# Performance work log

Hardware: AMD Instinct MI355X
Metric: run time of the kernel (lower is better)

The kernel has to match this reference:

```python
import jax, jax.numpy as jnp
import numpy as np

EPS = 1e-5  # torch LayerNorm default

def _std(x):
    # standardize over the last 3 (tensor-feature) modes, biased variance like torch LayerNorm
    mu = jnp.mean(x, axis=(-3, -2, -1), keepdims=True)
    var = jnp.mean(jnp.square(x - mu), axis=(-3, -2, -1), keepdims=True)
    return (x - mu) * jax.lax.rsqrt(var + EPS)

def setup_inputs() -> dict:
    key = jax.random.key(0)
    ks = jax.random.split(key, 12)
    T, B = 512, 16
    a = b = c = 16          # input tensor modes (4096 features)
    ha = hb = hc = 8        # hidden tensor modes (512 features)
    G = 3                   # gates: r, z, n
    f32 = jnp.float32
    return {
        "x": jax.random.normal(ks[0], (T, B, a, b, c), f32),
        "h0": jnp.zeros((B, ha, hb, hc), f32),
        # input-to-hidden TCL3D factors + rank-1 bias + LN affines (stacked over 3 gates)
        "W_fa": jax.random.normal(ks[1], (G, a, ha), f32),
        "W_fb": jax.random.normal(ks[2], (G, b, hb), f32),
        "W_fc": jax.random.normal(ks[3], (G, c, hc), f32),
        "W_ba": jax.random.normal(ks[4], (G, ha), f32),
        "W_bb": jax.random.normal(ks[5], (G, hb), f32),
        "W_bc": jax.random.normal(ks[6], (G, hc), f32),
        "W_lnin_w": jnp.ones((G, a, b, c), f32),
        "W_lnin_b": jnp.zeros((G, a, b, c), f32),
        "W_lnout_w": jnp.ones((G, ha, hb, hc), f32),
        "W_lnout_b": jnp.zeros((G, ha, hb, hc), f32),
        # hidden-to-hidden TCL3D factors + rank-1 bias + LN affines
        "U_fa": jax.random.normal(ks[7], (G, ha, ha), f32),
        "U_fb": jax.random.normal(ks[8], (G, hb, hb), f32),
        "U_fc": jax.random.normal(ks[9], (G, hc, hc), f32),
        "U_ba": jax.random.normal(ks[10], (G, ha), f32),
        "U_bb": jax.random.normal(ks[11], (G, hb), f32),
        "U_bc": jax.random.normal(jax.random.fold_in(key, 99), (G, hc), f32),
        "U_lnin_w": jnp.ones((G, ha, hb, hc), f32),
        "U_lnin_b": jnp.zeros((G, ha, hb, hc), f32),
        "U_lnout_w": jnp.ones((G, ha, hb, hc), f32),
        "U_lnout_b": jnp.zeros((G, ha, hb, hc), f32),
    }

def reference(x, h0, W_fa, W_fb, W_fc, W_ba, W_bb, W_bc,
              W_lnin_w, W_lnin_b, W_lnout_w, W_lnout_b,
              U_fa, U_fb, U_fc, U_ba, U_bb, U_bc,
              U_lnin_w, U_lnin_b, U_lnout_w, U_lnout_b):
    # --- input-to-hidden TCL3D for all 3 gates, batched over time (no h dependence) ---
    xh = _std(x)                                                  # [T,B,a,b,c]
    xg = xh[None] * W_lnin_w[:, None, None] + W_lnin_b[:, None, None]  # [3,T,B,a,b,c]
    Wx = jnp.einsum('gtnabc,gad,gbe,gcf->gtndef', xg, W_fa, W_fb, W_fc)
    Wx = Wx + (W_ba[:, None, None, :, None, None]
               * W_bb[:, None, None, None, :, None]
               * W_bc[:, None, None, None, None, :])              # rank-1 bias
    Wx = _std(Wx) * W_lnout_w[:, None, None] + W_lnout_b[:, None, None]
    Wx = jnp.swapaxes(Wx, 0, 1)                                   # [T,3,B,ha,hb,hc]

    Ub = (U_ba[:, None, :, None, None]
          * U_bb[:, None, None, :, None]
          * U_bc[:, None, None, None, :])                         # [3,1,ha,hb,hc]

    def step(h, wx):
        # hidden-to-hidden TCL3D for all 3 gates
        hh = _std(h)                                              # [B,ha,hb,hc]
        hg = hh[None] * U_lnin_w[:, None] + U_lnin_b[:, None]     # [3,B,ha,hb,hc]
        Uh = jnp.einsum('gndef,gdp,geq,gfr->gnpqr', hg, U_fa, U_fb, U_fc) + Ub
        Uh = _std(Uh) * U_lnout_w[:, None] + U_lnout_b[:, None]
        r = jax.nn.sigmoid(wx[0] + Uh[0])
        z = jax.nn.sigmoid(wx[1] + Uh[1])
        n = jnp.tanh(wx[2] + r * Uh[2])
        h_new = (1.0 - z) * n + z * h
        return h_new, h_new

    _, outs = jax.lax.scan(step, h0, Wx)                          # [T,B,ha,hb,hc]
    return outs
```

## Files before the change

### kernel.cpp

```cpp
#include <hip/hip_runtime.h>

#define EPSV 1e-5f

#define DPP_XADD(v, ctrl)                                                  \
    v += __int_as_float(__builtin_amdgcn_update_dpp(                       \
        0, __float_as_int(v), ctrl, 0xF, 0xF, false))

__device__ __forceinline__ float wave_allsum(float v) {
    DPP_XADD(v, 0x128);
    DPP_XADD(v, 0x124);
    DPP_XADD(v, 0x122);
    DPP_XADD(v, 0x121);
    DPP_XADD(v, 0x142);
    DPP_XADD(v, 0x143);
    return __int_as_float(__builtin_amdgcn_readlane(__float_as_int(v), 63));
}

__global__ __launch_bounds__(256) void wx_kernel(
    const float* __restrict__ x,
    const float* __restrict__ Wfa, const float* __restrict__ Wfb,
    const float* __restrict__ Wfc,
    const float* __restrict__ Wba, const float* __restrict__ Wbb,
    const float* __restrict__ Wbc,
    const float* __restrict__ lniw, const float* __restrict__ lnib,
    const float* __restrict__ lnow, const float* __restrict__ lnob,
    float* __restrict__ wxo)
{
    __shared__ float Xs[4096];
    __shared__ float S1[2048];
    __shared__ float S2[1024];
    __shared__ float baS[24], bbS[24], bcS[24];
    __shared__ float red[16];

    const int tid  = threadIdx.x;
    const int wid  = tid >> 6, lane = tid & 63;
    const size_t tb = blockIdx.x;
    const float* xp = x + tb * 4096;

    float s = 0.f, s2 = 0.f;
    for (int i = tid; i < 4096; i += 256) {
        float v = xp[i];
        Xs[i] = v;
        s += v; s2 += v * v;
    }
    if (tid < 24) { baS[tid] = Wba[tid]; bbS[tid] = Wbb[tid]; bcS[tid] = Wbc[tid]; }

    __syncthreads();
    #pragma unroll
    for (int off = 32; off > 0; off >>= 1) {
        s  += __shfl_down(s,  off);
        s2 += __shfl_down(s2, off);
    }
    if (lane == 0) { red[wid] = s; red[8 + wid] = s2; }
    __syncthreads();
    s  = red[0] + red[1] + red[2] + red[3];
    s2 = red[8] + red[9] + red[10] + red[11];
    const float muX = s * (1.f / 4096.f);
    const float rsX = rsqrtf(fmaxf(s2 * (1.f / 4096.f) - muX * muX, 0.f) + EPSV);

    const int qh = __builtin_amdgcn_readfirstlane(tid >> 7);
    const int rh = __builtin_amdgcn_readfirstlane(tid >> 6);

    for (int g = 0; g < 3; ++g) {
        {
            float acc[8] = {0,0,0,0,0,0,0,0};
            const int rest = tid;
            const float* lw = lniw + g * 4096;
            const float* lb = lnib + g * 4096;
            #pragma unroll
            for (int m = 0; m < 16; ++m) {
                const float xn = (Xs[m*256 + rest] - muX) * rsX;
                const float xv = fmaf(xn, lw[m*256 + rest], lb[m*256 + rest]);
                #pragma unroll
                for (int p = 0; p < 8; ++p)
                    acc[p] = fmaf(xv, Wfa[(g*16 + m)*8 + p], acc[p]);
            }
            #pragma unroll
            for (int p = 0; p < 8; ++p)
                S1[p*256 + (rest ^ (p << 3))] = acc[p];
        }
        __syncthreads();
        {
            float acc[4] = {0,0,0,0};
            const int rest2 = tid & 127;
            const int c2 = rest2 >> 3, p2 = rest2 & 7;
            #pragma unroll
            for (int m = 0; m < 16; ++m) {
                const float xv = S1[p2*256 + (((m << 4) | c2) ^ (p2 << 3))];
                #pragma unroll
                for (int j = 0; j < 4; ++j)
                    acc[j] = fmaf(xv, Wfb[(g*16 + m)*8 + qh*4 + j], acc[j]);
            }
            #pragma unroll
            for (int j = 0; j < 4; ++j) {
                const int q = qh*4 + j;
                S2[q*128 + (rest2 ^ (q << 3))] = acc[j];
            }
        }
        __syncthreads();
        float v0, v1; int idx0;
        {
            float acc[2] = {0, 0};
            const int rest3 = tid & 63;
            const int q3 = rest3 & 7, pp = rest3 >> 3;
            #pragma unroll
            for (int m = 0; m < 16; ++m) {
                const float xv = S2[q3*128 + (((m << 3) | pp) ^ (q3 << 3))];
                #pragma unroll
                for (int j = 0; j < 2; ++j)
                    acc[j] = fmaf(xv, Wfc[(g*16 + m)*8 + rh*2 + j], acc[j]);
            }
            const float bpq = baS[g*8 + pp] * bbS[g*8 + q3];
            v0 = acc[0] + bpq * bcS[g*8 + rh*2 + 0];
            v1 = acc[1] + bpq * bcS[g*8 + rh*2 + 1];
            idx0 = rest3 * 8 + rh * 2;
        }
        float t = v0 + v1, t2 = v0*v0 + v1*v1;
        __syncthreads();
        #pragma unroll
        for (int off = 32; off > 0; off >>= 1) {
            t  += __shfl_down(t,  off);
            t2 += __shfl_down(t2, off);
        }
        if (lane == 0) { red[wid] = t; red[8 + wid] = t2; }
        __syncthreads();
        t  = red[0] + red[1] + red[2] + red[3];
        t2 = red[8] + red[9] + red[10] + red[11];
        const float mu  = t * (1.f / 512.f);
        const float var = fmaxf(t2 * (1.f / 512.f) - mu * mu, 0.f);
        const float rs  = rsqrtf(var + EPSV);
        float* wp = wxo + (tb * 3 + g) * 512;
        const float2 lw2 = *(const float2*)(lnow + g*512 + idx0);
        const float2 lb2 = *(const float2*)(lnob + g*512 + idx0);
        float2 o2;
        o2.x = fmaf((v0 - mu) * rs, lw2.x, lb2.x);
        o2.y = fmaf((v1 - mu) * rs, lw2.y, lb2.y);
        *(float2*)(wp + idx0) = o2;
    }
}

__global__ __launch_bounds__(192, 1) void scan_kernel(
    const float* __restrict__ wx,
    const float* __restrict__ h0,
    const float* __restrict__ Ufa, const float* __restrict__ Ufb,
    const float* __restrict__ Ufc,
    const float* __restrict__ Uba, const float* __restrict__ Ubb,
    const float* __restrict__ Ubc,
    const float* __restrict__ lniw, const float* __restrict__ lnib,
    const float* __restrict__ lnow, const float* __restrict__ lnob,
    float* __restrict__ out,
    int T, int B)
{
    const int n    = blockIdx.x;
    const int tid  = threadIdx.x;
    const int lane = tid & 63;
    const int gu   = __builtin_amdgcn_readfirstlane(tid >> 6);

    __shared__ float hgS[3][512];
    __shared__ float T1S[3][512];
    __shared__ float T2S[3][512];
    __shared__ float UhS[2][3][512];

    const float* __restrict__ WA = Ufa + gu * 64;
    const float* __restrict__ WB = Ufb + gu * 64;
    const float* __restrict__ WC = Ufc + gu * 64;

    float lnw[8], lnb[8], low8[8], lob8[8], ub[8];
    {
        const int p_ = lane >> 3, q_ = lane & 7;
        const float bpq = Uba[gu*8 + p_] * Ubb[gu*8 + q_];
        #pragma unroll
        for (int k = 0; k < 8; ++k) {
            lnw[k]  = lniw[gu*512 + lane*8 + k];
            lnb[k]  = lnib[gu*512 + lane*8 + k];
            low8[k] = lnow[gu*512 + lane*8 + k];
            lob8[k] = lnob[gu*512 + lane*8 + k];
            ub[k]   = bpq * Ubc[gu*8 + k];
        }
    }

    int wb[8], rb2[8];
    #pragma unroll
    for (int j = 0; j < 8; ++j) wb[j] = j*64 + (lane ^ (j << 2));
    {
        const int c = lane & 7, r = lane >> 3;
        #pragma unroll
        for (int m = 0; m < 8; ++m)
            rb2[m] = c*64 + (((m << 3) | r) ^ (c << 2));
    }

    float hv[8];
    {
        const float4 a = *(const float4*)(h0 + n*512 + lane*8);
        const float4 b = *(const float4*)(h0 + n*512 + lane*8 + 4);
        hv[0]=a.x; hv[1]=a.y; hv[2]=a.z; hv[3]=a.w;
        hv[4]=b.x; hv[5]=b.y; hv[6]=b.z; hv[7]=b.w;
    }

    float pf[3][8];
#define LOADWX(TT)                                                         \
    {                                                                      \
        const float* base_ = wx + (((size_t)(TT) * B + n) * 3) * 512       \
                             + lane * 8;                                   \
        _Pragma("unroll")                                                  \
        for (int gg = 0; gg < 3; ++gg) {                                   \
            const float4 A_ = *(const float4*)(base_ + gg*512);            \
            const float4 B_ = *(const float4*)(base_ + gg*512 + 4);       \
            pf[gg][0]=A_.x; pf[gg][1]=A_.y; pf[gg][2]=A_.z; pf[gg][3]=A_.w;\
            pf[gg][4]=B_.x; pf[gg][5]=B_.y; pf[gg][6]=B_.z; pf[gg][7]=B_.w;\
        }                                                                  \
    }

#define STAGE(INBUF, WPTR, AOUT)                                           \
    _Pragma("unroll")                                                      \
    for (int m = 0; m < 8; ++m) {                                          \
        const float xv = INBUF[gu][rb2[m]];                                \
        _Pragma("unroll")                                                  \
        for (int q = 0; q < 8; ++q)                                        \
            AOUT[q] = fmaf(xv, WPTR[m*8 + q], AOUT[q]);                    \
    }

#define PIPELINE(PAR)                                                      \
    {                                                                      \
        float sA = 0.f, sB = 0.f;                                          \
        _Pragma("unroll")                                                  \
        for (int k = 0; k < 8; ++k) { sA += hv[k]; sB += hv[k]*hv[k]; }    \
        sA = wave_allsum(sA); sB = wave_allsum(sB);                        \
        const float mu_ = sA * (1.f/512.f);                                \
        const float rs_ = rsqrtf(fmaxf(sB*(1.f/512.f) - mu_*mu_, 0.f)      \
                                 + EPSV);                                  \
        _Pragma("unroll")                                                  \
        for (int k = 0; k < 8; ++k)                                        \
            hgS[gu][wb[k]] = fmaf((hv[k]-mu_)*rs_, lnw[k], lnb[k]);        \
        float a_[8];                                                       \
        _Pragma("unroll") for (int k = 0; k < 8; ++k) a_[k] = 0.f;         \
        STAGE(hgS, WA, a_)                                                 \
        _Pragma("unroll")                                                  \
        for (int k = 0; k < 8; ++k) { T1S[gu][wb[k]] = a_[k]; a_[k] = 0.f;}\
        STAGE(T1S, WB, a_)                                                 \
        _Pragma("unroll")                                                  \
        for (int k = 0; k < 8; ++k) { T2S[gu][wb[k]] = a_[k]; a_[k] = 0.f;}\
        STAGE(T2S, WC, a_)                                                 \
        float sC = 0.f, sD = 0.f;                                          \
        _Pragma("unroll")                                                  \
        for (int k = 0; k < 8; ++k) {                                      \
            a_[k] += ub[k]; sC += a_[k]; sD += a_[k]*a_[k];                \
        }                                                                  \
        sC = wave_allsum(sC); sD = wave_allsum(sD);                        \
        const float mu2_ = sC * (1.f/512.f);                               \
        const float rs2_ = rsqrtf(fmaxf(sD*(1.f/512.f) - mu2_*mu2_, 0.f)   \
                                  + EPSV);                                 \
        _Pragma("unroll")                                                  \
        for (int k = 0; k < 8; ++k)                                        \
            UhS[PAR][gu][wb[k]] = fmaf((a_[k]-mu2_)*rs2_, low8[k],         \
                                       lob8[k]);                           \
    }

#define COMBINE(PAR)                                                       \
    {                                                                      \
        float u0[8], u1[8], u2[8];                                         \
        _Pragma("unroll")                                                  \
        for (int k = 0; k < 8; ++k) {                                      \
            u0[k] = UhS[PAR][0][wb[k]];                                    \
            u1[k] = UhS[PAR][1][wb[k]];                                    \
            u2[k] = UhS[PAR][2][wb[k]];                                    \
        }                                                                  \
        _Pragma("unroll")                                                  \
        for (int k = 0; k < 8; ++k) {                                      \
            const float er_ = __expf(-(pf[0][k] + u0[k]));                 \
            const float r_  = __builtin_amdgcn_rcpf(1.f + er_);            \
            const float ez_ = __expf(-(pf[1][k] + u1[k]));                 \
            const float z_  = __builtin_amdgcn_rcpf(1.f + ez_);            \
            const float e2_ = __expf(2.f*(pf[2][k] + r_*u2[k]));           \
            const float nn_ = 1.f - 2.f*__builtin_amdgcn_rcpf(e2_ + 1.f);  \
            hv[k] = (1.f - z_)*nn_ + z_*hv[k];                             \
        }                                                                  \
    }

    LOADWX(0);
    PIPELINE(0);

    for (int t = 0; t < T; ++t) {
        __syncthreads();
        COMBINE(t & 1);
        if (gu == 0) {
            float* op = out + ((size_t)t * B + n) * 512 + lane*8;
            *(float4*)op     = make_float4(hv[0], hv[1], hv[2], hv[3]);
            *(float4*)(op+4) = make_float4(hv[4], hv[5], hv[6], hv[7]);
        }
        if (t + 1 < T) {
            LOADWX(t + 1);
            PIPELINE((t + 1) & 1);
        }
    }
#undef LOADWX
#undef STAGE
#undef PIPELINE
#undef COMBINE
}

extern "C" void kernel_launch(void* const* d_in, const int* in_sizes, int n_in,
                              void* d_out, int out_size, void* d_ws, size_t ws_size,
                              hipStream_t stream)
{
    const float* x    = (const float*)d_in[0];
    const float* h0   = (const float*)d_in[1];
    const float* Wfa  = (const float*)d_in[2];
    const float* Wfb  = (const float*)d_in[3];
    const float* Wfc  = (const float*)d_in[4];
    const float* Wba  = (const float*)d_in[5];
    const float* Wbb  = (const float*)d_in[6];
    const float* Wbc  = (const float*)d_in[7];
    const float* Wliw = (const float*)d_in[8];
    const float* Wlib = (const float*)d_in[9];
    const float* Wlow = (const float*)d_in[10];
    const float* Wlob = (const float*)d_in[11];
    const float* Ufa  = (const float*)d_in[12];
    const float* Ufb  = (const float*)d_in[13];
    const float* Ufc  = (const float*)d_in[14];
    const float* Uba  = (const float*)d_in[15];
    const float* Ubb  = (const float*)d_in[16];
    const float* Ubc  = (const float*)d_in[17];
    const float* Uliw = (const float*)d_in[18];
    const float* Ulib = (const float*)d_in[19];
    const float* Ulow = (const float*)d_in[20];
    const float* Ulob = (const float*)d_in[21];

    const int B = in_sizes[1] / 512;
    const int T = in_sizes[0] / (B * 4096);

    float* wxws = (float*)d_ws;
    float* out  = (float*)d_out;

    wx_kernel<<<T * B, 256, 0, stream>>>(x, Wfa, Wfb, Wfc, Wba, Wbb, Wbc,
                                         Wliw, Wlib, Wlow, Wlob, wxws);
    scan_kernel<<<B, 192, 0, stream>>>(wxws, h0, Ufa, Ufb, Ufc, Uba, Ubb, Ubc,
                                       Uliw, Ulib, Ulow, Ulob, out, T, B);
}
```

Before: 933.2 us.

## Split gate combine across waves and share hidden state through LDS

The scan kernel now splits the GRU combine step across the three gate waves. Each wave computes 2-3 of the 8 elements per lane and writes the new hidden state into a shared LDS buffer, instead of every wave redundantly computing all 8 elements. Each wave then reads the hidden state back in the transposed layout, so the input LayerNorm folds directly into the first contraction stage and the hgS store/load round trip goes away. In exchange the loop needs two barriers per timestep instead of one and loses the double-buffered Uh. The wx prefetch becomes scalar per-element loads rather than float4 loads.

After: 1.068 ms. 14.4% more time.

```diff
diff --git a/kernel.cpp b/kernel.cpp
--- a/kernel.cpp
+++ b/kernel.cpp
@@ -156,26 +156,26 @@
     const int lane = tid & 63;
     const int gu   = __builtin_amdgcn_readfirstlane(tid >> 6);
 
-    __shared__ float hgS[3][512];
+    __shared__ float hS[512];
     __shared__ float T1S[3][512];
     __shared__ float T2S[3][512];
-    __shared__ float UhS[2][3][512];
+    __shared__ float UhS[3][512];
 
     const float* __restrict__ WA = Ufa + gu * 64;
     const float* __restrict__ WB = Ufb + gu * 64;
     const float* __restrict__ WC = Ufc + gu * 64;
 
-    float lnw[8], lnb[8], low8[8], lob8[8], ub[8];
+    float lnwT[8], lnbT[8], low8[8], lob8[8], ubias[8];
     {
         const int p_ = lane >> 3, q_ = lane & 7;
         const float bpq = Uba[gu*8 + p_] * Ubb[gu*8 + q_];
         #pragma unroll
         for (int k = 0; k < 8; ++k) {
-            lnw[k]  = lniw[gu*512 + lane*8 + k];
-            lnb[k]  = lnib[gu*512 + lane*8 + k];
-            low8[k] = lnow[gu*512 + lane*8 + k];
-            lob8[k] = lnob[gu*512 + lane*8 + k];
-            ub[k]   = bpq * Ubc[gu*8 + k];
+            lnwT[k]  = lniw[gu*512 + k*64 + lane];
+            lnbT[k]  = lnib[gu*512 + k*64 + lane];
+            low8[k]  = lnow[gu*512 + lane*8 + k];
+            lob8[k]  = lnob[gu*512 + lane*8 + k];
+            ubias[k] = bpq * Ubc[gu*8 + k];
         }
     }
 
@@ -189,114 +189,136 @@
             rb2[m] = c*64 + (((m << 3) | r) ^ (c << 2));
     }
 
-    float hv[8];
-    {
-        const float4 a = *(const float4*)(h0 + n*512 + lane*8);
-        const float4 b = *(const float4*)(h0 + n*512 + lane*8 + 4);
-        hv[0]=a.x; hv[1]=a.y; hv[2]=a.z; hv[3]=a.w;
-        hv[4]=b.x; hv[5]=b.y; hv[6]=b.z; hv[7]=b.w;
-    }
-
-    float pf[3][8];
-#define LOADWX(TT)                                                         \
+    float hold[3];
+    float pf[3][3];
+    float uo[8];
+
+#define LOADWX_SLICE(TT, K0, KN)                                           \
     {                                                                      \
-        const float* base_ = wx + (((size_t)(TT) * B + n) * 3) * 512       \
-                             + lane * 8;                                   \
+        const float* b_ = wx + ((size_t)(TT) * B + n) * 1536 + lane * 8;   \
         _Pragma("unroll")                                                  \
-        for (int gg = 0; gg < 3; ++gg) {                                   \
-            const float4 A_ = *(const float4*)(base_ + gg*512);            \
-            const float4 B_ = *(const float4*)(base_ + gg*512 + 4);       \
-            pf[gg][0]=A_.x; pf[gg][1]=A_.y; pf[gg][2]=A_.z; pf[gg][3]=A_.w;\
-            pf[gg][4]=B_.x; pf[gg][5]=B_.y; pf[gg][6]=B_.z; pf[gg][7]=B_.w;\
-        }                                                                  \
-    }
-
-#define STAGE(INBUF, WPTR, AOUT)                                           \
-    _Pragma("unroll")                                                      \
-    for (int m = 0; m < 8; ++m) {                                          \
-        const float xv = INBUF[gu][rb2[m]];                                \
-        _Pragma("unroll")                                                  \
-        for (int q = 0; q < 8; ++q)                                        \
-            AOUT[q] = fmaf(xv, WPTR[m*8 + q], AOUT[q]);                    \
-    }
-
-#define PIPELINE(PAR)                                                      \
+        for (int gg = 0; gg < 3; ++gg)                                     \
+            _Pragma("unroll")                                              \
+            for (int kk = 0; kk < (KN); ++kk)                              \
+                pf[gg][kk] = b_[gg*512 + (K0) + kk];                       \
+    }
+
+#define CMB(K, KK, E_UR, E_UZ, E_UN)                                       \
     {                                                                      \
-        float sA = 0.f, sB = 0.f;                                          \
-        _Pragma("unroll")                                                  \
-        for (int k = 0; k < 8; ++k) { sA += hv[k]; sB += hv[k]*hv[k]; }    \
-        sA = wave_allsum(sA); sB = wave_allsum(sB);                        \
-        const float mu_ = sA * (1.f/512.f);                                \
-        const float rs_ = rsqrtf(fmaxf(sB*(1.f/512.f) - mu_*mu_, 0.f)      \
-                                 + EPSV);                                  \
-        _Pragma("unroll")                                                  \
-        for (int k = 0; k < 8; ++k)                                        \
-            hgS[gu][wb[k]] = fmaf((hv[k]-mu_)*rs_, lnw[k], lnb[k]);        \
-        float a_[8];                                                       \
-        _Pragma("unroll") for (int k = 0; k < 8; ++k) a_[k] = 0.f;         \
-        STAGE(hgS, WA, a_)                                                 \
-        _Pragma("unroll")                                                  \
-        for (int k = 0; k < 8; ++k) { T1S[gu][wb[k]] = a_[k]; a_[k] = 0.f;}\
-        STAGE(T1S, WB, a_)                                                 \
-        _Pragma("unroll")                                                  \
-        for (int k = 0; k < 8; ++k) { T2S[gu][wb[k]] = a_[k]; a_[k] = 0.f;}\
-        STAGE(T2S, WC, a_)                                                 \
-        float sC = 0.f, sD = 0.f;                                          \
-        _Pragma("unroll")                                                  \
-        for (int k = 0; k < 8; ++k) {                                      \
-            a_[k] += ub[k]; sC += a_[k]; sD += a_[k]*a_[k];                \
-        }                                                                  \
-        sC = wave_allsum(sC); sD = wave_allsum(sD);                        \
-        const float mu2_ = sC * (1.f/512.f);                               \
-        const float rs2_ = rsqrtf(fmaxf(sD*(1.f/512.f) - mu2_*mu2_, 0.f)   \
-                                  + EPSV);                                 \
-        _Pragma("unroll")                                                  \
-        for (int k = 0; k < 8; ++k)                                        \
-            UhS[PAR][gu][wb[k]] = fmaf((a_[k]-mu2_)*rs2_, low8[k],         \
-                                       lob8[k]);                           \
-    }
-
-#define COMBINE(PAR)                                                       \
-    {                                                                      \
-        float u0[8], u1[8], u2[8];                                         \
-        _Pragma("unroll")                                                  \
-        for (int k = 0; k < 8; ++k) {                                      \
-            u0[k] = UhS[PAR][0][wb[k]];                                    \
-            u1[k] = UhS[PAR][1][wb[k]];                                    \
-            u2[k] = UhS[PAR][2][wb[k]];                                    \
-        }                                                                  \
-        _Pragma("unroll")                                                  \
-        for (int k = 0; k < 8; ++k) {                                      \
-            const float er_ = __expf(-(pf[0][k] + u0[k]));                 \
-            const float r_  = __builtin_amdgcn_rcpf(1.f + er_);            \
-            const float ez_ = __expf(-(pf[1][k] + u1[k]));                 \
-            const float z_  = __builtin_amdgcn_rcpf(1.f + ez_);            \
-            const float e2_ = __expf(2.f*(pf[2][k] + r_*u2[k]));           \
-            const float nn_ = 1.f - 2.f*__builtin_amdgcn_rcpf(e2_ + 1.f);  \
-            hv[k] = (1.f - z_)*nn_ + z_*hv[k];                             \
-        }                                                                  \
-    }
-
-    LOADWX(0);
-    PIPELINE(0);
+        const float ur_ = (E_UR), uz_ = (E_UZ), un_ = (E_UN);              \
+        const float er_ = __expf(-(pf[0][KK] + ur_));                      \
+        const float r_  = __builtin_amdgcn_rcpf(1.f + er_);                \
+        const float ez_ = __expf(-(pf[1][KK] + uz_));                      \
+        const float z_  = __builtin_amdgcn_rcpf(1.f + ez_);                \
+        const float e2_ = __expf(2.f * (pf[2][KK] + r_ * un_));            \
+        const float nn_ = 1.f - 2.f * __builtin_amdgcn_rcpf(e2_ + 1.f);    \
+        const float hn_ = (1.f - z_) * nn_ + z_ * hold[KK];                \
+        hold[KK] = hn_;                                                    \
+        op_[K]   = hn_;                                                    \
+        hS[wb[K]] = hn_;                                                   \
+    }
+
+    if (gu == 0) {
+        #pragma unroll
+        for (int kk = 0; kk < 3; ++kk) {
+            hold[kk] = h0[n*512 + lane*8 + kk];
+            hS[wb[kk]] = hold[kk];
+        }
+        LOADWX_SLICE(0, 0, 3)
+    } else if (gu == 1) {
+        #pragma unroll
+        for (int kk = 0; kk < 3; ++kk) {
+            hold[kk] = h0[n*512 + lane*8 + 3 + kk];
+            hS[wb[3 + kk]] = hold[kk];
+        }
+        LOADWX_SLICE(0, 3, 3)
+    } else {
+        #pragma unroll
+        for (int kk = 0; kk < 2; ++kk) {
+            hold[kk] = h0[n*512 + lane*8 + 6 + kk];
+            hS[wb[6 + kk]] = hold[kk];
+        }
+        LOADWX_SLICE(0, 6, 2)
+    }
+    __syncthreads();
 
     for (int t = 0; t < T; ++t) {
-        __syncthreads();
-        COMBINE(t & 1);
-        if (gu == 0) {
-            float* op = out + ((size_t)t * B + n) * 512 + lane*8;
-            *(float4*)op     = make_float4(hv[0], hv[1], hv[2], hv[3]);
-            *(float4*)(op+4) = make_float4(hv[4], hv[5], hv[6], hv[7]);
-        }
-        if (t + 1 < T) {
-            LOADWX(t + 1);
-            PIPELINE((t + 1) & 1);
-        }
-    }
-#undef LOADWX
-#undef STAGE
-#undef PIPELINE
-#undef COMBINE
+        {
+            float xv[8];
+            #pragma unroll
+            for (int m = 0; m < 8; ++m) xv[m] = hS[rb2[m]];
+            float sA = 0.f, sB = 0.f;
+            #pragma unroll
+            for (int m = 0; m < 8; ++m) { sA += xv[m]; sB += xv[m]*xv[m]; }
+            sA = wave_allsum(sA); sB = wave_allsum(sB);
+            const float mu_ = sA * (1.f/512.f);
+            const float rs_ = rsqrtf(fmaxf(sB*(1.f/512.f) - mu_*mu_, 0.f)
+                                     + EPSV);
+            float a_[8] = {0,0,0,0,0,0,0,0};
+            #pragma unroll
+            for (int m = 0; m < 8; ++m) {
+                const float xg = fmaf((xv[m]-mu_)*rs_, lnwT[m], lnbT[m]);
+                #pragma unroll
+                for (int q = 0; q < 8; ++q)
+                    a_[q] = fmaf(xg, WA[m*8 + q], a_[q]);
+            }
+            #pragma unroll
+            for (int k = 0; k < 8; ++k) { T1S[gu][wb[k]] = a_[k]; a_[k] = 0.f; }
+            #pragma unroll
+            for (int m = 0; m < 8; ++m) {
+                const float xv2 = T1S[gu][rb2[m]];
+                #pragma unroll
+                for (int q = 0; q < 8; ++q)
+                    a_[q] = fmaf(xv2, WB[m*8 + q], a_[q]);
+            }
+            #pragma unroll
+            for (int k = 0; k < 8; ++k) { T2S[gu][wb[k]] = a_[k]; a_[k] = 0.f; }
+            #pragma unroll
+            for (int m = 0; m < 8; ++m) {
+                const float xv3 = T2S[gu][rb2[m]];
+                #pragma unroll
+                for (int q = 0; q < 8; ++q)
+                    a_[q] = fmaf(xv3, WC[m*8 + q], a_[q]);
+            }
+            float sC = 0.f, sD = 0.f;
+            #pragma unroll
+            for (int k = 0; k < 8; ++k) {
+                a_[k] += ubias[k]; sC += a_[k]; sD += a_[k]*a_[k];
+            }
+            sC = wave_allsum(sC); sD = wave_allsum(sD);
+            const float mu2_ = sC * (1.f/512.f);
+            const float rs2_ = rsqrtf(fmaxf(sD*(1.f/512.f) - mu2_*mu2_, 0.f)
+                                      + EPSV);
+            #pragma unroll
+            for (int k = 0; k < 8; ++k) {
+                uo[k] = fmaf((a_[k]-mu2_)*rs2_, low8[k], lob8[k]);
+                UhS[gu][wb[k]] = uo[k];
+            }
+        }
+        __syncthreads();
+
+        {
+            float* op_ = out + ((size_t)t * B + n) * 512 + lane*8;
+            if (gu == 0) {
+                CMB(0, 0, uo[0], UhS[1][wb[0]], UhS[2][wb[0]])
+                CMB(1, 1, uo[1], UhS[1][wb[1]], UhS[2][wb[1]])
+                CMB(2, 2, uo[2], UhS[1][wb[2]], UhS[2][wb[2]])
+                if (t + 1 < T) LOADWX_SLICE(t + 1, 0, 3)
+            } else if (gu == 1) {
+                CMB(3, 0, UhS[0][wb[3]], uo[3], UhS[2][wb[3]])
+                CMB(4, 1, UhS[0][wb[4]], uo[4], UhS[2][wb[4]])
+                CMB(5, 2, UhS[0][wb[5]], uo[5], UhS[2][wb[5]])
+                if (t + 1 < T) LOADWX_SLICE(t + 1, 3, 3)
+            } else {
+                CMB(6, 0, UhS[0][wb[6]], UhS[1][wb[6]], uo[6])
+                CMB(7, 1, UhS[0][wb[7]], UhS[1][wb[7]], uo[7])
+                if (t + 1 < T) LOADWX_SLICE(t + 1, 6, 2)
+            }
+        }
+        __syncthreads();
+    }
+#undef LOADWX_SLICE
+#undef CMB
 }
 
 extern "C" void kernel_launch(void* const* d_in, const int* in_sizes, int n_in,
```
